# Kernel tuning notes

Measured on AMD Instinct MI355X. Metric: run time of the kernel, lower is better.

Reference implementation:

```python
import jax, jax.numpy as jnp
import numpy as np

N = 100000      # nodes
E = 1600000     # edges (before self-loops)
IN = 256        # input features
HID = 128       # hidden channels
HEADS = 8
C = HID // HEADS  # per-head channels = 16
L = 3           # num GAT layers
EPS = 1e-5      # batchnorm eps
NEG_SLOPE = 0.2 # leaky relu slope (PyG GATConv default)


def setup_inputs() -> dict:
    key = jax.random.key(0)
    ks = jax.random.split(key, 8)
    s = 0.05
    x = jax.random.normal(ks[0], (N, IN), jnp.float32)
    edge_index = jax.random.randint(ks[1], (2, E), 0, N, dtype=jnp.int32)
    proj_w = jax.random.normal(ks[2], (IN, HID), jnp.float32) * s
    proj_b = jnp.zeros((HID,), jnp.float32)
    W = jax.random.normal(ks[3], (L, HID, HID), jnp.float32) * s
    att_src = jax.random.normal(ks[4], (L, HEADS, C), jnp.float32) * s
    att_dst = jax.random.normal(ks[5], (L, HEADS, C), jnp.float32) * s
    conv_b = jnp.zeros((L, HID), jnp.float32)
    bn_g = jnp.ones((L, HID), jnp.float32)
    bn_b = jnp.zeros((L, HID), jnp.float32)
    fc_w = jax.random.normal(ks[6], (HID, 1), jnp.float32) * s
    fc_b = jnp.zeros((1,), jnp.float32)
    return {"x": x, "edge_index": edge_index, "proj_w": proj_w, "proj_b": proj_b,
            "W": W, "att_src": att_src, "att_dst": att_dst, "conv_b": conv_b,
            "bn_g": bn_g, "bn_b": bn_b, "fc_w": fc_w, "fc_b": fc_b}


def _gat_layer(x, src, dst, W, a_src, a_dst, b):
    # x: [N, HID] -> per-head features h: [N, HEADS, C]
    h = (x @ W).reshape(N, HEADS, C)
    al_src = jnp.einsum('nhc,hc->nh', h, a_src)  # [N, HEADS]
    al_dst = jnp.einsum('nhc,hc->nh', h, a_dst)  # [N, HEADS]
    e = jax.nn.leaky_relu(al_src[src] + al_dst[dst], NEG_SLOPE)  # [Etot, HEADS]
    # segment softmax over edges grouped by destination node
    m = jax.ops.segment_max(e, dst, num_segments=N)              # [N, HEADS]
    w = jnp.exp(e - m[dst])
    denom = jax.ops.segment_sum(w, dst, num_segments=N)          # [N, HEADS]
    alpha = w / (denom[dst] + 1e-16)                             # [Etot, HEADS]
    msg = h[src] * alpha[:, :, None]                             # [Etot, HEADS, C]
    out = jax.ops.segment_sum(msg, dst, num_segments=N)          # [N, HEADS, C]
    return out.reshape(N, HID) + b


def reference(x, edge_index, proj_w, proj_b, W, att_src, att_dst, conv_b, bn_g, bn_b, fc_w, fc_b):
    # add self loops (PyG GATConv default)
    loops = jnp.arange(N, dtype=edge_index.dtype)
    src = jnp.concatenate([edge_index[0], loops])
    dst = jnp.concatenate([edge_index[1], loops])
    h = jax.nn.elu(x @ proj_w + proj_b)
    for i in range(L):
        res = h
        h = _gat_layer(h, src, dst, W[i], att_src[i], att_dst[i], conv_b[i])
        mu = h.mean(axis=0)
        var = h.var(axis=0)  # biased, matches torch BN training math
        h = (h - mu) / jnp.sqrt(var + EPS) * bn_g[i] + bn_b[i]
        h = jax.nn.elu(h)
        h = h + res  # residual; dropout is identity in eval mode
    return h @ fc_w + fc_b
```

## Files before the change

### kernel.cpp

```cpp
#include <hip/hip_runtime.h>
#include <hip/hip_bf16.h>

#define NN 100000
#define EE 1600000
#define ETOT (NN + EE)
#define HID 128
#define HEADS 8
#define CH 16
#define EPS_BN 1e-5f
#define NEG_SLOPE 0.2f
#define LOG2E 1.4426950408889634f
#define NB 196
#define NBLK_A 208

typedef unsigned short ushort_t;
typedef unsigned int uint_t;
typedef __attribute__((ext_vector_type(8))) short short8;
typedef __attribute__((ext_vector_type(4))) float float4v;

__device__ inline uint_t f2bf(float x) {
    __hip_bfloat16 b = __float2bfloat16(x);
    return (uint_t)*reinterpret_cast<unsigned short*>(&b);
}
__device__ inline uint_t pack2(float lo, float hi) {
    return f2bf(lo) | (f2bf(hi) << 16);
}
__device__ inline float bf_lo(uint_t u) { return __uint_as_float(u << 16); }
__device__ inline float bf_hi(uint_t u) { return __uint_as_float(u & 0xffff0000u); }


__global__ __launch_bounds__(256) void bucket_hist(const int* __restrict__ ei,
                                                   int* bcnt, int* lbase) {
    __shared__ int h[256];
    int t = threadIdx.x;
    h[t] = 0;
    __syncthreads();
    int base = blockIdx.x * 8192;
    #pragma unroll 4
    for (int j = 0; j < 32; ++j) {
        int i = base + j * 256 + t;
        if (i < ETOT) {
            int d = (i < EE) ? ei[EE + i] : (i - EE);
            atomicAdd(&h[d >> 9], 1);
        }
    }
    __syncthreads();
    if (t < NB) {
        int v = h[t];
        lbase[blockIdx.x * NB + t] = v ? atomicAdd(&bcnt[t], v) : 0;
    }
}

__global__ void bucket_scan(const int* __restrict__ bcnt, int* bbase, int* rowptr) {
    __shared__ int s[256];
    int t = threadIdx.x;
    int orig = (t < NB) ? bcnt[t] : 0;
    s[t] = orig;
    __syncthreads();
    for (int off = 1; off < 256; off <<= 1) {
        int add = (t >= off) ? s[t - off] : 0;
        __syncthreads();
        s[t] += add;
        __syncthreads();
    }
    if (t < NB) bbase[t] = s[t] - orig;
    if (t == 0) { bbase[NB] = ETOT; rowptr[NN] = ETOT; }
}

__global__ __launch_bounds__(256) void bucket_scatter(const int* __restrict__ ei,
                                                      const int* __restrict__ bbase,
                                                      const int* __restrict__ lbase,
                                                      uint_t* __restrict__ pairs) {
    __shared__ uint_t spair[8192];
    __shared__ unsigned char sbk[8192];
    __shared__ int h[256];
    __shared__ int lscan[256];
    __shared__ int sbase[256];
    int t = threadIdx.x;
    int base = blockIdx.x * 8192;
    int nloc = ETOT - base; if (nloc > 8192) nloc = 8192;
    sbase[t] = (t < NB) ? (bbase[t] + lbase[blockIdx.x * NB + t]) : 0;
    h[t] = 0;
    __syncthreads();
    #pragma unroll 4
    for (int j = 0; j < 32; ++j) {
        int i = base + j * 256 + t;
        if (i < ETOT) {
            int d = (i < EE) ? ei[EE + i] : (i - EE);
            atomicAdd(&h[d >> 9], 1);
        }
    }
    __syncthreads();
    int orig = h[t];
    lscan[t] = orig;
    __syncthreads();
    for (int off = 1; off < 256; off <<= 1) {
        int add = (t >= off) ? lscan[t - off] : 0;
        __syncthreads();
        lscan[t] += add;
        __syncthreads();
    }
    int excl = lscan[t] - orig;
    __syncthreads();
    lscan[t] = excl;
    h[t] = excl;
    __syncthreads();
    #pragma unroll 4
    for (int j = 0; j < 32; ++j) {
        int i = base + j * 256 + t;
        if (i < ETOT) {
            int sv, dv;
            if (i < EE) { sv = ei[i]; dv = ei[EE + i]; }
            else        { sv = i - EE; dv = sv; }
            int bk = dv >> 9;
            int lp = atomicAdd(&h[bk], 1);
            spair[lp] = ((uint_t)sv << 9) | (uint_t)(dv & 511);
            sbk[lp] = (unsigned char)bk;
        }
    }
    __syncthreads();
    #pragma unroll 4
    for (int j = 0; j < 32; ++j) {
        int i = j * 256 + t;
        if (i < nloc) {
            int bk = sbk[i];
            pairs[sbase[bk] + (i - lscan[bk])] = spair[i];
        }
    }
}

__global__ __launch_bounds__(256) void bucket_build(const uint_t* __restrict__ pairs,
                                                    const int* __restrict__ bbase,
                                                    int* __restrict__ rowptr,
                                                    int* __restrict__ csrc) {
    __shared__ int cnt[512];
    __shared__ int cur[512];
    int b = blockIdx.x;
    int t = threadIdx.x;
    int lo = b << 9;
    int nn = NN - lo; if (nn > 512) nn = 512;
    int e0 = bbase[b];
    int e1 = bbase[b + 1];
    cnt[t] = 0; cnt[t + 256] = 0;
    __syncthreads();
    for (int i = e0 + t; i < e1; i += 256)
        atomicAdd(&cnt[pairs[i] & 511], 1);
    __syncthreads();
    int oc0 = cnt[t], oc1 = cnt[t + 256];
    for (int off = 1; off < 512; off <<= 1) {
        int i0 = t, i1 = t + 256;
        int a0 = cnt[i0] + ((i0 >= off) ? cnt[i0 - off] : 0);
        int a1 = cnt[i1] + ((i1 >= off) ? cnt[i1 - off] : 0);
        __syncthreads();
        cnt[i0] = a0; cnt[i1] = a1;
        __syncthreads();
    }
    int ex0 = cnt[t] - oc0, ex1 = cnt[t + 256] - oc1;
    __syncthreads();
    cur[t] = e0 + ex0; cur[t + 256] = e0 + ex1;
    if (t < nn)       rowptr[lo + t] = e0 + ex0;
    if (t + 256 < nn) rowptr[lo + 256 + t] = e0 + ex1;
    __syncthreads();
    for (int i = e0 + t; i < e1; i += 256) {
        uint_t p = pairs[i];
        int pos = atomicAdd(&cur[p & 511], 1);
        csrc[pos] = (int)(p >> 9);
    }
}


__global__ void castw(const float* __restrict__ proj_w, const float* __restrict__ W,
                      ushort_t* __restrict__ pwT, ushort_t* __restrict__ WT,
                      int* __restrict__ zbuf) {
    int id = blockIdx.x * 256 + threadIdx.x;
    if (id < 1024) zbuf[id] = 0;
    if (id < 32768) {
        int n = id >> 8, k = id & 255;
        pwT[id] = (ushort_t)f2bf(proj_w[k * 128 + n]);
    } else if (id < 81920) {
        int id2 = id - 32768;
        int l = id2 >> 14, r = id2 & 16383;
        int n = r >> 7, k = r & 127;
        WT[id2] = (ushort_t)f2bf(W[l * 16384 + k * 128 + n]);
    }
}


__global__ __launch_bounds__(256) void gemm_mfma(
    const void* __restrict__ Aptr, int mode,
    const ushort_t* __restrict__ Bt, int K,
    const float* __restrict__ bias, ushort_t* __restrict__ Cb,
    const float* __restrict__ a_src, const float* __restrict__ a_dst,
    float* __restrict__ al_s, float* __restrict__ al_d, int M,
    uint_t* __restrict__ hbio, const float* __restrict__ stats,
    const float* __restrict__ bn_gl, const float* __restrict__ bn_bl)
{
    __shared__ uint4 smem[2304];
    __shared__ float2 scsh[128];
    ushort_t* As = (ushort_t*)smem;
    ushort_t* Bs = As + 128 * 72;

    int t = threadIdx.x;
    int row0 = blockIdx.x * 128;
    int lane = t & 63, wv = t >> 6;
    int wm = wv >> 1, wn = wv & 1;
    int lr = lane & 15, quad = lane >> 4;

    if (mode == 2 && t < 128) {
        float mu = stats[t] * (1.0f / NN);
        float var = stats[128 + t] * (1.0f / NN) - mu * mu;
        float s = bn_gl[t] * rsqrtf(var + EPS_BN);
        scsh[t] = make_float2(s, bn_bl[t] - mu * s);
    }
    __syncthreads();

    float4v acc[4][4] = {};

    for (int k0 = 0; k0 < K; k0 += 64) {
        if (mode == 1) {
            const float* A = (const float*)Aptr;
            #pragma unroll
            for (int j = 0; j < 8; ++j) {
                int idx = j * 256 + t;
                int row = idx >> 4;
                int c4 = (idx & 15) * 4;
                int gr = row0 + row;
                float4 v = make_float4(0.f, 0.f, 0.f, 0.f);
                if (gr < M) v = *(const float4*)(A + (size_t)gr * K + k0 + c4);
                uint2 u; u.x = pack2(v.x, v.y); u.y = pack2(v.z, v.w);
                *(uint2*)&As[row * 72 + c4] = u;
            }
        } else if (mode == 0) {
            const ushort_t* A = (const ushort_t*)Aptr;
            #pragma unroll
            for (int j = 0; j < 4; ++j) {
                int idx = j * 256 + t;
                int row = idx >> 3;
                int c8 = (idx & 7) * 8;
                int gr = row0 + row;
                uint4 v = make_uint4(0, 0, 0, 0);
                if (gr < M) v = *(const uint4*)(A + (size_t)gr * K + k0 + c8);
                *(uint4*)&As[row * 72 + c8] = v;
            }
        } else {
            const uint_t* agg = (const uint_t*)Aptr;
            #pragma unroll
            for (int j = 0; j < 4; ++j) {
                int idx = j * 256 + t;
                int row = idx >> 3;
                int u4 = idx & 7;
                int gr = row0 + row;
                uint4 o = make_uint4(0, 0, 0, 0);
                if (gr < M) {
                    size_t gi = (size_t)gr * 64 + (k0 >> 1) + u4 * 4;
                    uint4 av = *(const uint4*)(agg + gi);
                    uint4 rv = *(const uint4*)(hbio + gi);
                    int cb = k0 + u4 * 8;
                    uint_t aa[4] = {av.x, av.y, av.z, av.w};
                    uint_t rr[4] = {rv.x, rv.y, rv.z, rv.w};
                    float ov[8];
                    #pragma unroll
                    for (int q = 0; q < 4; ++q) {
                        float2 s0 = scsh[cb + 2 * q];
                        float2 s1 = scsh[cb + 2 * q + 1];
                        float x0 = s0.x * bf_lo(aa[q]) + s0.y;
                        x0 = x0 > 0.f ? x0 : __expf(x0) - 1.f;
                        x0 += bf_lo(rr[q]);
                        float x1 = s1.x * bf_hi(aa[q]) + s1.y;
                        x1 = x1 > 0.f ? x1 : __expf(x1) - 1.f;
                        x1 += bf_hi(rr[q]);
                        ov[2 * q] = x0; ov[2 * q + 1] = x1;
                    }
                    o.x = pack2(ov[0], ov[1]); o.y = pack2(ov[2], ov[3]);
                    o.z = pack2(ov[4], ov[5]); o.w = pack2(ov[6], ov[7]);
                    *(uint4*)(hbio + gi) = o;
                }
                *(uint4*)&As[row * 72 + u4 * 8] = o;
            }
        }
        #pragma unroll
        for (int j = 0; j < 4; ++j) {
            int idx = j * 256 + t;
            int row = idx >> 3;
            int c8 = (idx & 7) * 8;
            uint4 v = *(const uint4*)(Bt + (size_t)row * K + k0 + c8);
            *(uint4*)&Bs[row * 72 + c8] = v;
        }
        __syncthreads();

        const ushort_t* Ab = As + (wm * 64 + lr) * 72 + quad * 8;
        const ushort_t* Bb = Bs + (wn * 64 + lr) * 72 + quad * 8;
        #pragma unroll
        for (int ks = 0; ks < 64; ks += 32) {
            short8 a[4], b[4];
            #pragma unroll
            for (int ti = 0; ti < 4; ++ti) a[ti] = *(const short8*)(Ab + ti * 16 * 72 + ks);
            #pragma unroll
            for (int tj = 0; tj < 4; ++tj) b[tj] = *(const short8*)(Bb + tj * 16 * 72 + ks);
            #pragma unroll
            for (int ti = 0; ti < 4; ++ti)
                #pragma unroll
                for (int tj = 0; tj < 4; ++tj)
                    acc[ti][tj] = __builtin_amdgcn_mfma_f32_16x16x32_bf16(
                        a[ti], b[tj], acc[ti][tj], 0, 0, 0);
        }
        __syncthreads();
    }

    float* sc = (float*)smem;
    for (int tp = 0; tp < 2; ++tp) {
        #pragma unroll
        for (int th = 0; th < 2; ++th) {
            int ti = tp * 2 + th;
            #pragma unroll
            for (int tj = 0; tj < 4; ++tj) {
                #pragma unroll
                for (int r = 0; r < 4; ++r) {
                    int rloc = wm * 32 + th * 16 + quad * 4 + r;
                    int col = wn * 64 + tj * 16 + lr;
                    sc[rloc * 132 + col] = acc[ti][tj][r];
                }
            }
        }
        __syncthreads();
        #pragma unroll
        for (int j = 0; j < 8; ++j) {
            int idx = j * 256 + t;
            int row = idx >> 5;
            int c4 = (idx & 31) * 4;
            float4 v = *(const float4*)&sc[row * 132 + c4];
            int gr = row0 + (row >> 5) * 64 + tp * 32 + (row & 31);
            if (gr < M) {
                if (bias) {
                    float4 bv = *(const float4*)(bias + c4);
                    v.x += bv.x; v.y += bv.y; v.z += bv.z; v.w += bv.w;
                    v.x = v.x > 0.f ? v.x : __expf(v.x) - 1.f;
                    v.y = v.y > 0.f ? v.y : __expf(v.y) - 1.f;
                    v.z = v.z > 0.f ? v.z : __expf(v.z) - 1.f;
                    v.w = v.w > 0.f ? v.w : __expf(v.w) - 1.f;
                }
                uint2 u; u.x = pack2(v.x, v.y); u.y = pack2(v.z, v.w);
                *(uint2*)(Cb + (size_t)gr * 128 + c4) = u;
            }
        }
        if (al_s) {
            #pragma unroll
            for (int jj = 0; jj < 2; ++jj) {
                int task = jj * 256 + t;
                int row = task & 63, head = task >> 6;
                int gr = row0 + (row >> 5) * 64 + tp * 32 + (row & 31);
                if (gr < M) {
                    const float* rp = &sc[row * 132 + head * 16];
                    const float* spv = a_src + head * 16;
                    const float* dpv = a_dst + head * 16;
                    float s1 = 0.f, s2 = 0.f;
                    #pragma unroll
                    for (int c = 0; c < 16; ++c) {
                        float hv = rp[c];
                        s1 += hv * spv[c];
                        s2 += hv * dpv[c];
                    }
                    al_s[gr * 8 + head] = s1 * LOG2E;
                    al_d[gr * 8 + head] = s2 * LOG2E;
                }
            }
        }
        __syncthreads();
    }
}


__global__ __launch_bounds__(256) void gat_agg(
    const int* __restrict__ rowptr, const int* __restrict__ csrc,
    const uint4* __restrict__ h2b4, const float* __restrict__ al_s,
    const float* __restrict__ al_d, const float* __restrict__ bias,
    uint4* __restrict__ out4)
{
    int wv = (blockIdx.x * blockDim.x + threadIdx.x) >> 6;
    int lane = threadIdx.x & 63;
    if (wv >= NN) return;
    int slot = lane >> 4;
    int ln = lane & 15;
    int head = ln >> 1;
    const char* hb8 = (const char*)h2b4;
    const char* as8 = (const char*)al_s;
    unsigned hoff = (unsigned)ln * 16u;
    unsigned aoff = (unsigned)head * 4u;
    int e0 = rowptr[wv], e1 = rowptr[wv + 1];
    float ald = al_d[(unsigned)wv * 8u + head];
    float ac[8] = {};
    float denom = 0.f;

    int e = e0;
    for (; e + 16 <= e1; e += 16) {
        int sA = csrc[e + slot];
        int sB = csrc[e + 4 + slot];
        int sC = csrc[e + 8 + slot];
        int sD = csrc[e + 12 + slot];
        float aA = *(const float*)(as8 + ((unsigned)sA * 32u + aoff));
        float aB = *(const float*)(as8 + ((unsigned)sB * 32u + aoff));
        float aC = *(const float*)(as8 + ((unsigned)sC * 32u + aoff));
        float aD = *(const float*)(as8 + ((unsigned)sD * 32u + aoff));
        uint4 pA = *(const uint4*)(hb8 + ((unsigned)sA * 256u + hoff));
        uint4 pB = *(const uint4*)(hb8 + ((unsigned)sB * 256u + hoff));
        uint4 pC = *(const uint4*)(hb8 + ((unsigned)sC * 256u + hoff));
        uint4 pD = *(const uint4*)(hb8 + ((unsigned)sD * 256u + hoff));
        float xA = aA + ald; xA = fmaxf(xA, NEG_SLOPE * xA); float wA = exp2f(xA);
        float xB = aB + ald; xB = fmaxf(xB, NEG_SLOPE * xB); float wB = exp2f(xB);
        float xC = aC + ald; xC = fmaxf(xC, NEG_SLOPE * xC); float wC = exp2f(xC);
        float xD = aD + ald; xD = fmaxf(xD, NEG_SLOPE * xD); float wD = exp2f(xD);
        uint_t uA[4] = {pA.x, pA.y, pA.z, pA.w};
        uint_t uB[4] = {pB.x, pB.y, pB.z, pB.w};
        uint_t uC[4] = {pC.x, pC.y, pC.z, pC.w};
        uint_t uD[4] = {pD.x, pD.y, pD.z, pD.w};
        #pragma unroll
        for (int q = 0; q < 4; ++q) {
            ac[2 * q]     += wA * bf_lo(uA[q]) + wB * bf_lo(uB[q])
                           + wC * bf_lo(uC[q]) + wD * bf_lo(uD[q]);
            ac[2 * q + 1] += wA * bf_hi(uA[q]) + wB * bf_hi(uB[q])
                           + wC * bf_hi(uC[q]) + wD * bf_hi(uD[q]);
        }
        denom += (wA + wB) + (wC + wD);
    }
    for (; e + 8 <= e1; e += 8) {
        int sA = csrc[e + slot];
        int sB = csrc[e + 4 + slot];
        float aA = *(const float*)(as8 + ((unsigned)sA * 32u + aoff));
        float aB = *(const float*)(as8 + ((unsigned)sB * 32u + aoff));
        uint4 pA = *(const uint4*)(hb8 + ((unsigned)sA * 256u + hoff));
        uint4 pB = *(const uint4*)(hb8 + ((unsigned)sB * 256u + hoff));
        float xA = aA + ald; xA = fmaxf(xA, NEG_SLOPE * xA);
        float wA = exp2f(xA);
        float xB = aB + ald; xB = fmaxf(xB, NEG_SLOPE * xB);
        float wB = exp2f(xB);
        uint_t uA[4] = {pA.x, pA.y, pA.z, pA.w};
        uint_t uB[4] = {pB.x, pB.y, pB.z, pB.w};
        #pragma unroll
        for (int q = 0; q < 4; ++q) {
            ac[2 * q]     += wA * bf_lo(uA[q]) + wB * bf_lo(uB[q]);
            ac[2 * q + 1] += wA * bf_hi(uA[q]) + wB * bf_hi(uB[q]);
        }
        denom += wA + wB;
    }
    for (; e < e1; e += 4) {
        int idx = e + slot;
        bool valid = idx < e1;
        int s = csrc[valid ? idx : e];
        float a = *(const float*)(as8 + ((unsigned)s * 32u + aoff));
        uint4 p = *(const uint4*)(hb8 + ((unsigned)s * 256u + hoff));
        float x = a + ald; x = fmaxf(x, NEG_SLOPE * x);
        float w = valid ? exp2f(x) : 0.f;
        uint_t u[4] = {p.x, p.y, p.z, p.w};
        #pragma unroll
        for (int q = 0; q < 4; ++q) {
            ac[2 * q]     += w * bf_lo(u[q]);
            ac[2 * q + 1] += w * bf_hi(u[q]);
        }
        denom += w;
    }
    #pragma unroll
    for (int q = 0; q < 8; ++q) {
        ac[q] += __shfl_xor(ac[q], 16, 64);
        ac[q] += __shfl_xor(ac[q], 32, 64);
    }
    denom += __shfl_xor(denom, 16, 64);
    denom += __shfl_xor(denom, 32, 64);
    if (slot == 0) {
        float inv = 1.0f / (denom + 1e-16f);
        int c = ln * 8;
        float4 b0 = *(const float4*)(bias + c);
        float4 b1 = *(const float4*)(bias + c + 4);
        uint4 o;
        o.x = pack2(ac[0] * inv + b0.x, ac[1] * inv + b0.y);
        o.y = pack2(ac[2] * inv + b0.z, ac[3] * inv + b0.w);
        o.z = pack2(ac[4] * inv + b1.x, ac[5] * inv + b1.y);
        o.w = pack2(ac[6] * inv + b1.z, ac[7] * inv + b1.w);
        out4[(size_t)wv * 16 + ln] = o;
    }
}


__global__ void bn_stats(const uint_t* __restrict__ ab, float* stats) {
    int t = threadIdx.x;
    int u_idx = t >> 1, hi = t & 1;
    float s = 0.f, q = 0.f;
    for (int r0 = blockIdx.x * 4; r0 < NN; r0 += gridDim.x * 4) {
        #pragma unroll
        for (int j = 0; j < 4; ++j) {
            int r = r0 + j;
            if (r < NN) {
                uint_t u = ab[(size_t)r * 64 + u_idx];
                float v = hi ? bf_hi(u) : bf_lo(u);
                s += v;
                q += v * v;
            }
        }
    }
    atomicAdd(&stats[t], s);
    atomicAdd(&stats[HID + t], q);
}


__global__ __launch_bounds__(256) void fc_fused(
    const uint_t* __restrict__ aggb, const uint_t* __restrict__ hb,
    const float* __restrict__ stats, const float* __restrict__ g,
    const float* __restrict__ be, const float* __restrict__ w,
    const float* __restrict__ fb, float* __restrict__ out)
{
    __shared__ float2 scsh[128];
    int t = threadIdx.x;
    if (t < 128) {
        float mu = stats[t] * (1.0f / NN);
        float var = stats[128 + t] * (1.0f / NN) - mu * mu;
        float s = g[t] * rsqrtf(var + EPS_BN);
        scsh[t] = make_float2(s, be[t] - mu * s);
    }
    __syncthreads();
    int wv = (blockIdx.x * 256 + t) >> 6;
    int lane = t & 63;
    if (wv >= NN) return;
    uint_t av = aggb[(size_t)wv * 64 + lane];
    uint_t rv = hb[(size_t)wv * 64 + lane];
    int c = lane * 2;
    float2 s0 = scsh[c], s1 = scsh[c + 1];
    float x0 = s0.x * bf_lo(av) + s0.y;
    x0 = x0 > 0.f ? x0 : __expf(x0) - 1.f;
    x0 += bf_lo(rv);
    float x1 = s1.x * bf_hi(av) + s1.y;
    x1 = x1 > 0.f ? x1 : __expf(x1) - 1.f;
    x1 += bf_hi(rv);
    float2 wl = *(const float2*)(w + c);
    float acc = x0 * wl.x + x1 * wl.y;
    #pragma unroll
    for (int off = 32; off > 0; off >>= 1)
        acc += __shfl_down(acc, off, 64);
    if (lane == 0) out[wv] = acc + fb[0];
}


extern "C" void kernel_launch(void* const* d_in, const int* in_sizes, int n_in,
                              void* d_out, int out_size, void* d_ws, size_t ws_size,
                              hipStream_t stream) {
    const float* x       = (const float*)d_in[0];
    const int*   ei      = (const int*)  d_in[1];
    const float* proj_w  = (const float*)d_in[2];
    const float* proj_b  = (const float*)d_in[3];
    const float* W       = (const float*)d_in[4];
    const float* att_src = (const float*)d_in[5];
    const float* att_dst = (const float*)d_in[6];
    const float* conv_b  = (const float*)d_in[7];
    const float* bn_g    = (const float*)d_in[8];
    const float* bn_b    = (const float*)d_in[9];
    const float* fc_w    = (const float*)d_in[10];
    const float* fc_b    = (const float*)d_in[11];
    float* out = (float*)d_out;

    char* p = (char*)d_ws;
    uint_t*   hb   = (uint_t*)p;   p += (size_t)NN * 64 * 4;
    uint_t*   h2b  = (uint_t*)p;   p += (size_t)NN * 64 * 4;
    uint_t*   aggb = (uint_t*)p;   p += (size_t)NN * 64 * 4;
    uint_t*   pairs = (uint_t*)aggb;
    float*    al_s = (float*)p;    p += (size_t)NN * HEADS * 4;
    float*    al_d = (float*)p;    p += (size_t)NN * HEADS * 4;
    int* rowptr    = (int*)p;      p += ((size_t)(NN + 1) * 4 + 255) & ~255ull;
    int* csrc      = (int*)p;      p += (size_t)ETOT * 4;
    int* bcnt      = (int*)p;      p += 1024;
    float* stats3  = (float*)p;    p += 3 * 1024;
    int* bbase     = (int*)p;      p += 1024;
    int* lbase     = (int*)p;      p += (size_t)NBLK_A * NB * 4 + 256;
    ushort_t* pwT  = (ushort_t*)p; p += 128 * 256 * 2;
    ushort_t* WT   = (ushort_t*)p; p += 3 * 128 * 128 * 2;
    (void)ws_size; (void)n_in; (void)in_sizes; (void)out_size;

    castw<<<320, 256, 0, stream>>>(proj_w, W, pwT, WT, bcnt);

    gemm_mfma<<<(NN + 127) / 128, 256, 0, stream>>>(
        x, 1, pwT, 256, proj_b, (ushort_t*)hb, nullptr, nullptr, nullptr, nullptr, NN,
        nullptr, nullptr, nullptr, nullptr);

    bucket_hist<<<NBLK_A, 256, 0, stream>>>(ei, bcnt, (int*)lbase);
    bucket_scan<<<1, 256, 0, stream>>>(bcnt, bbase, rowptr);
    bucket_scatter<<<NBLK_A, 256, 0, stream>>>(ei, bbase, (const int*)lbase, pairs);
    bucket_build<<<NB, 256, 0, stream>>>(pairs, bbase, rowptr, csrc);

    for (int l = 0; l < 3; ++l) {
        const ushort_t* WTl = WT + (size_t)l * 128 * 128;
        const float* asl = att_src + (size_t)l * HEADS * CH;
        const float* adl = att_dst + (size_t)l * HEADS * CH;
        const float* cbl = conv_b + (size_t)l * HID;
        float* stl = stats3 + l * 256;

        if (l == 0) {
            gemm_mfma<<<(NN + 127) / 128, 256, 0, stream>>>(
                hb, 0, WTl, 128, nullptr, (ushort_t*)h2b, asl, adl, al_s, al_d, NN,
                nullptr, nullptr, nullptr, nullptr);
        } else {
            gemm_mfma<<<(NN + 127) / 128, 256, 0, stream>>>(
                aggb, 2, WTl, 128, nullptr, (ushort_t*)h2b, asl, adl, al_s, al_d, NN,
                hb, stats3 + (l - 1) * 256, bn_g + (size_t)(l - 1) * HID,
                bn_b + (size_t)(l - 1) * HID);
        }
        gat_agg<<<(NN + 3) / 4, 256, 0, stream>>>(
            rowptr, csrc, (const uint4*)h2b, al_s, al_d, cbl, (uint4*)aggb);
        bn_stats<<<512, 128, 0, stream>>>(aggb, stl);
    }

    fc_fused<<<(NN + 3) / 4, 256, 0, stream>>>(
        aggb, hb, stats3 + 2 * 256, bn_g + 2 * HID, bn_b + 2 * HID, fc_w, fc_b, out);
}
```

Measured before the change: 809.9 us.

## Add specialized K=128 layer GEMM with direct global-to-LDS loads

Adds a dedicated layer_gemm kernel for the three 128x128 per-layer GEMMs, replacing the generic gemm_mfma. It loads the whole K=128 tiles of A and B into LDS at once, using global_load_lds for the B tile and, in mode 0, the A tile. In mode 2 it applies the fused BN, ELU and residual while staging A. The epilogue writes bf16 output and computes the attention logits from LDS. The goal is to cut the generic kernel's K-loop and register staging overhead, at the cost of more LDS per block, which may reduce occupancy.

```diff
diff --git a/kernel.cpp b/kernel.cpp
--- a/kernel.cpp
+++ b/kernel.cpp
@@ -27,6 +27,12 @@
 }
 __device__ inline float bf_lo(uint_t u) { return __uint_as_float(u << 16); }
 __device__ inline float bf_hi(uint_t u) { return __uint_as_float(u & 0xffff0000u); }
+
+__device__ inline void gld_lds16(const void* g, void* l) {
+    __builtin_amdgcn_global_load_lds(
+        (const __attribute__((address_space(1))) unsigned int*)g,
+        (__attribute__((address_space(3))) unsigned int*)l, 16, 0, 0);
+}
 
 
 __global__ __launch_bounds__(256) void bucket_hist(const int* __restrict__ ei,
@@ -370,6 +376,175 @@
 }
 
 
+__global__ __launch_bounds__(256) void layer_gemm(
+    const void* __restrict__ Aptr, int mode,
+    const ushort_t* __restrict__ Bt, ushort_t* __restrict__ Cb,
+    const float* __restrict__ a_src, const float* __restrict__ a_dst,
+    float* __restrict__ al_s, float* __restrict__ al_d,
+    uint_t* __restrict__ hbio, const float* __restrict__ stats,
+    const float* __restrict__ bn_gl, const float* __restrict__ bn_bl)
+{
+    __shared__ uint4 smem[4096];
+    __shared__ float2 scsh[128];
+    ushort_t* As = (ushort_t*)smem;
+    ushort_t* Bs = As + 16384;
+
+    int t = threadIdx.x;
+    int row0 = blockIdx.x * 128;
+    int lane = t & 63, wv = t >> 6;
+    int wm = wv >> 1, wn = wv & 1;
+    int lr = lane & 15, quad = lane >> 4;
+
+    if (mode == 2) {
+        if (t < 128) {
+            float mu = stats[t] * (1.0f / NN);
+            float var = stats[128 + t] * (1.0f / NN) - mu * mu;
+            float s = bn_gl[t] * rsqrtf(var + EPS_BN);
+            scsh[t] = make_float2(s, bn_bl[t] - mu * s);
+        }
+        __syncthreads();
+    }
+
+    #pragma unroll
+    for (int j = 0; j < 8; ++j) {
+        int idx = j * 256 + t;
+        int tile = idx >> 8, ksf = (idx >> 6) & 3;
+        int l = idx & 63;
+        int n = tile * 16 + (l & 15);
+        int kk = ksf * 32 + (l >> 4) * 8;
+        gld_lds16(Bt + n * 128 + kk, Bs + (size_t)idx * 8);
+    }
+
+    if (mode == 0) {
+        const ushort_t* A = (const ushort_t*)Aptr;
+        #pragma unroll
+        for (int j = 0; j < 8; ++j) {
+            int idx = j * 256 + t;
+            int tile = idx >> 8, ksf = (idx >> 6) & 3;
+            int l = idx & 63;
+            int row = row0 + tile * 16 + (l & 15);
+            int kk = ksf * 32 + (l >> 4) * 8;
+            gld_lds16(A + (size_t)row * 128 + kk, As + (size_t)idx * 8);
+        }
+    } else {
+        const uint_t* agg = (const uint_t*)Aptr;
+        uint4 av[8], rv[8];
+        unsigned gi[8];
+        int rowv[8];
+        #pragma unroll
+        for (int j = 0; j < 8; ++j) {
+            int idx = j * 256 + t;
+            int tile = idx >> 8, ksf = (idx >> 6) & 3;
+            int l = idx & 63;
+            int row = row0 + tile * 16 + (l & 15);
+            int kk = ksf * 32 + (l >> 4) * 8;
+            unsigned ui = (unsigned)row * 64u + (unsigned)(kk >> 1);
+            gi[j] = ui; rowv[j] = row;
+            av[j] = *(const uint4*)(agg + ui);
+            rv[j] = *(const uint4*)(hbio + ui);
+        }
+        #pragma unroll
+        for (int j = 0; j < 8; ++j) {
+            int idx = j * 256 + t;
+            int ksf = (idx >> 6) & 3;
+            int l = idx & 63;
+            int kk = ksf * 32 + (l >> 4) * 8;
+            uint_t aa[4] = {av[j].x, av[j].y, av[j].z, av[j].w};
+            uint_t rr[4] = {rv[j].x, rv[j].y, rv[j].z, rv[j].w};
+            float ov[8];
+            #pragma unroll
+            for (int q = 0; q < 4; ++q) {
+                float2 s0 = scsh[kk + 2 * q];
+                float2 s1 = scsh[kk + 2 * q + 1];
+                float x0 = s0.x * bf_lo(aa[q]) + s0.y;
+                x0 = x0 > 0.f ? x0 : __expf(x0) - 1.f;
+                x0 += bf_lo(rr[q]);
+                float x1 = s1.x * bf_hi(aa[q]) + s1.y;
+                x1 = x1 > 0.f ? x1 : __expf(x1) - 1.f;
+                x1 += bf_hi(rr[q]);
+                ov[2 * q] = x0; ov[2 * q + 1] = x1;
+            }
+            uint4 o;
+            o.x = pack2(ov[0], ov[1]); o.y = pack2(ov[2], ov[3]);
+            o.z = pack2(ov[4], ov[5]); o.w = pack2(ov[6], ov[7]);
+            *(uint4*)(As + (size_t)idx * 8) = o;
+            if (rowv[j] < NN) *(uint4*)(hbio + gi[j]) = o;
+        }
+    }
+    __syncthreads();
+
+    float4v acc[4][4] = {};
+    #pragma unroll
+    for (int ks = 0; ks < 4; ++ks) {
+        short8 a[4], b[4];
+        #pragma unroll
+        for (int tj = 0; tj < 4; ++tj)
+            b[tj] = *(const short8*)(Bs + ((wn * 4 + tj) * 4 + ks) * 512 + lane * 8);
+        #pragma unroll
+        for (int ti = 0; ti < 4; ++ti)
+            a[ti] = *(const short8*)(As + ((wm * 4 + ti) * 4 + ks) * 512 + lane * 8);
+        #pragma unroll
+        for (int ti = 0; ti < 4; ++ti)
+            #pragma unroll
+            for (int tj = 0; tj < 4; ++tj)
+                acc[ti][tj] = __builtin_amdgcn_mfma_f32_16x16x32_bf16(
+                    a[ti], b[tj], acc[ti][tj], 0, 0, 0);
+    }
+    __syncthreads();
+
+    float* sc = (float*)smem;
+    for (int tp = 0; tp < 2; ++tp) {
+        #pragma unroll
+        for (int th = 0; th < 2; ++th) {
+            int ti = tp * 2 + th;
+            #pragma unroll
+            for (int tj = 0; tj < 4; ++tj) {
+                #pragma unroll
+                for (int r = 0; r < 4; ++r) {
+                    int rloc = wm * 32 + th * 16 + quad * 4 + r;
+                    int col = wn * 64 + tj * 16 + lr;
+                    sc[rloc * 132 + col] = acc[ti][tj][r];
+                }
+            }
+        }
+        __syncthreads();
+        #pragma unroll
+        for (int j = 0; j < 8; ++j) {
+            int idx = j * 256 + t;
+            int row = idx >> 5;
+            int c4 = (idx & 31) * 4;
+            float4 v = *(const float4*)&sc[row * 132 + c4];
+            int gr = row0 + (row >> 5) * 64 + tp * 32 + (row & 31);
+            if (gr < NN) {
+                uint2 u; u.x = pack2(v.x, v.y); u.y = pack2(v.z, v.w);
+                *(uint2*)(Cb + (size_t)gr * 128 + c4) = u;
+            }
+        }
+        #pragma unroll
+        for (int jj = 0; jj < 2; ++jj) {
+            int task = jj * 256 + t;
+            int row = task & 63, head = task >> 6;
+            int gr = row0 + (row >> 5) * 64 + tp * 32 + (row & 31);
+            if (gr < NN) {
+                const float* rp = &sc[row * 132 + head * 16];
+                const float* spv = a_src + head * 16;
+                const float* dpv = a_dst + head * 16;
+                float s1 = 0.f, s2 = 0.f;
+                #pragma unroll
+                for (int c = 0; c < 16; ++c) {
+                    float hv = rp[c];
+                    s1 += hv * spv[c];
+                    s2 += hv * dpv[c];
+                }
+                al_s[gr * 8 + head] = s1 * LOG2E;
+                al_d[gr * 8 + head] = s2 * LOG2E;
+            }
+        }
+        __syncthreads();
+    }
+}
+
+
 __global__ __launch_bounds__(256) void gat_agg(
     const int* __restrict__ rowptr, const int* __restrict__ csrc,
     const uint4* __restrict__ h2b4, const float* __restrict__ al_s,
@@ -591,12 +766,12 @@
         float* stl = stats3 + l * 256;
 
         if (l == 0) {
-            gemm_mfma<<<(NN + 127) / 128, 256, 0, stream>>>(
-                hb, 0, WTl, 128, nullptr, (ushort_t*)h2b, asl, adl, al_s, al_d, NN,
+            layer_gemm<<<(NN + 127) / 128, 256, 0, stream>>>(
+                hb, 0, WTl, (ushort_t*)h2b, asl, adl, al_s, al_d,
                 nullptr, nullptr, nullptr, nullptr);
         } else {
-            gemm_mfma<<<(NN + 127) / 128, 256, 0, stream>>>(
-                aggb, 2, WTl, 128, nullptr, (ushort_t*)h2b, asl, adl, al_s, al_d, NN,
+            layer_gemm<<<(NN + 127) / 128, 256, 0, stream>>>(
+                aggb, 2, WTl, (ushort_t*)h2b, asl, adl, al_s, al_d,
                 hb, stats3 + (l - 1) * 256, bn_g + (size_t)(l - 1) * HID,
                 bn_b + (size_t)(l - 1) * HID);
         }
```

Measured after the change: 804.6 us. No clear change (-0.7%).
